# Kernel optimization log

Measured on AMD Instinct MI355X. Metric: run time of the kernel, lower is better.

The kernel has to match this reference:

```python
import jax, jax.numpy as jnp
import numpy as np

H = 1024  # hidden_size


def _cell(x, W, b):
    # x: [S, B, D_in]; W: [4H, D_in]; b: [4H]
    # One big batched matmul over all timesteps (no recurrence exists).
    gates = jnp.einsum('sbd,gd->sbg', x, W) + b  # [S, B, 4H]
    i, f, g, o = jnp.split(gates, 4, axis=-1)
    i = jax.nn.sigmoid(i)
    g = jnp.tanh(g)
    o = jax.nn.sigmoid(o)
    c = i * g
    h = o * jnp.tanh(c)
    return h, c


def setup_inputs() -> dict:
    key = jax.random.key(0)
    ks = jax.random.split(key, 9)
    S, B, D = 2048, 8, 1024
    s = 1.0 / np.sqrt(D)
    s2 = 1.0 / np.sqrt(2 * H)
    return {
        'x': jax.random.normal(ks[0], (S, B, D), dtype=jnp.float32),
        'W_f0': jax.random.uniform(ks[1], (4 * H, D), jnp.float32, -s, s),
        'b_f0': jax.random.uniform(ks[2], (4 * H,), jnp.float32, -s, s),
        'W_b0': jax.random.uniform(ks[3], (4 * H, D), jnp.float32, -s, s),
        'b_b0': jax.random.uniform(ks[4], (4 * H,), jnp.float32, -s, s),
        'W_f1': jax.random.uniform(ks[5], (4 * H, 2 * H), jnp.float32, -s2, s2),
        'b_f1': jax.random.uniform(ks[6], (4 * H,), jnp.float32, -s2, s2),
        'W_b1': jax.random.uniform(ks[7], (4 * H, 2 * H), jnp.float32, -s2, s2),
        'b_b1': jax.random.uniform(ks[8], (4 * H,), jnp.float32, -s2, s2),
    }


def reference(x, W_f0, b_f0, W_b0, b_b0, W_f1, b_f1, W_b1, b_b1):
    out = x
    h_ns, c_ns = [], []
    for (Wf, bf, Wb, bb) in [(W_f0, b_f0, W_b0, b_b0), (W_f1, b_f1, W_b1, b_b1)]:
        h_f, c_f = _cell(out, Wf, bf)  # forward direction
        h_b, c_b = _cell(out, Wb, bb)  # backward direction (same per-t math)
        out = jnp.concatenate([h_f, h_b], axis=-1)  # [S, B, 2H]
        # forward final state is at t = S-1; backward final state at t = 0
        h_ns += [h_f[-1], h_b[0]]
        c_ns += [c_f[-1], c_b[0]]
    h_n = jnp.stack(h_ns, axis=0)  # [num_layers*2, B, H]
    c_n = jnp.stack(c_ns, axis=0)
    return out, h_n, c_n
```

## Files before the change

### kernel.cpp

```cpp
#include <hip/hip_runtime.h>
#include <hip/hip_bf16.h>

#define S_LEN 2048
#define BATCH 8
#define HID   1024
#define NP    3072
#define MROWS 16384

using bf16x8 = __attribute__((ext_vector_type(8))) short;
using f32x4  = __attribute__((ext_vector_type(4))) float;

__device__ __forceinline__ unsigned short f2b(float f) {
  unsigned int u = __builtin_bit_cast(unsigned int, f);
  u += 0x7fffu + ((u >> 16) & 1u);
  return (unsigned short)(u >> 16);
}

__device__ __forceinline__ void load_lds16(const void* g, void* l) {
  __builtin_amdgcn_global_load_lds(
      (const __attribute__((address_space(1))) void*)g,
      (__attribute__((address_space(3))) void*)(unsigned int)(unsigned long long)l,
      16, 0, 0);
}

#define MEMFENCE asm volatile("" ::: "memory")
#define BARRIER  do { MEMFENCE; __builtin_amdgcn_s_barrier(); MEMFENCE; } while (0)

__global__ void cvt_f32_bf16(const float* __restrict__ in,
                             unsigned short* __restrict__ out, int n4) {
  int i = blockIdx.x * blockDim.x + threadIdx.x;
  if (i >= n4) return;
  const float4 v = reinterpret_cast<const float4*>(in)[i];
  ushort4 u;
  u.x = f2b(v.x); u.y = f2b(v.y); u.z = f2b(v.z); u.w = f2b(v.w);
  reinterpret_cast<ushort4*>(out)[i] = u;
}

__global__ void permute_w(const float* __restrict__ W,
                          unsigned short* __restrict__ Wp, int K) {
  long i = ((long)blockIdx.x * blockDim.x + threadIdx.x) * 4;
  int np = (int)(i / K);
  if (np >= NP) return;
  int k0 = (int)(i % K);
  int chunk = np / 48, rem = np % 48;
  int g3 = rem >> 4, hl = rem & 15;
  int og = (g3 == 0) ? 0 : (g3 == 1) ? 2 : 3;
  int n  = og * 1024 + chunk * 16 + hl;
  const float4 v = *reinterpret_cast<const float4*>(W + (long)n * K + k0);
  ushort4 u;
  u.x = f2b(v.x); u.y = f2b(v.y); u.z = f2b(v.z); u.w = f2b(v.w);
  *reinterpret_cast<ushort4*>(Wp + i) = u;
}

__global__ void permute_b(const float* __restrict__ b, float* __restrict__ bp) {
  int np = blockIdx.x * blockDim.x + threadIdx.x;
  if (np >= NP) return;
  int chunk = np / 48, rem = np % 48;
  int g3 = rem >> 4, hl = rem & 15;
  int og = (g3 == 0) ? 0 : (g3 == 1) ? 2 : 3;
  bp[np] = b[og * 1024 + chunk * 16 + hl];
}

template <int MODE>
__global__ void __launch_bounds__(256, 2)
lstm_gemm(const unsigned short* __restrict__ A,
          const unsigned short* __restrict__ WpF,
          const unsigned short* __restrict__ WpB,
          const float* __restrict__ bpF, const float* __restrict__ bpB,
          int K,
          unsigned short* __restrict__ out_bf, float* __restrict__ out_f,
          float* __restrict__ hn, float* __restrict__ cn) {
  __shared__ __align__(16) char lds[81920];

  const int dir = blockIdx.z;
  const unsigned short* __restrict__ Wp = dir ? WpB : WpF;
  const float* __restrict__ bp = dir ? bpB : bpF;
  const int bm = blockIdx.y;
  const int bn = blockIdx.x;

  const int tid  = threadIdx.x;
  const int wid  = tid >> 6;
  const int lane = tid & 63;
  const int wm   = wid >> 1;
  const int wn   = wid & 1;

  const int  nt = K >> 6;
  const long K2 = (long)K * 2;

  const int rlane = lane >> 3;
  const int cb    = (((lane & 7) ^ rlane) << 4);
  const char* Asrc = (const char*)A  + ((long)bm * 128 + rlane) * K2 + cb;
  const char* Bsrc = (const char*)Wp + ((long)bn * 192 + rlane) * K2 + cb;

  const int l15 = lane & 15;
  const int hi  = lane >> 4;
  const int c0  = ((hi ^ (l15 & 7)) << 4);
  const int aro = (wm * 64 + l15) * 128;
  const int bro = 16384 + (wn * 96 + l15) * 128;

  f32x4 acc[4][6];
  const f32x4 zero = {0.f, 0.f, 0.f, 0.f};
#pragma unroll
  for (int i = 0; i < 4; ++i)
#pragma unroll
    for (int j = 0; j < 6; ++j) acc[i][j] = zero;

  auto STAGE = [&](int t) {
    if (t >= nt) return;
    char* d = lds + (t & 1) * 40960;
    const long off = (long)t * 128;
#pragma unroll
    for (int s = 0; s < 4; ++s) {
      const int slot = s * 4 + wid;
      load_lds16(Asrc + (long)(slot * 8) * K2 + off, d + slot * 1024);
    }
#pragma unroll
    for (int s = 0; s < 6; ++s) {
      const int slot = s * 4 + wid;
      load_lds16(Bsrc + (long)(slot * 8) * K2 + off, d + 16384 + slot * 1024);
    }
  };

  STAGE(0);
  asm volatile("s_waitcnt vmcnt(0)" ::: "memory");
  BARRIER;

  for (int t = 0; t < nt; ++t) {
    STAGE(t + 1);

    const char* buf = lds + (t & 1) * 40960;
    bf16x8 a[4][2], b[6][2];
#pragma unroll
    for (int nf = 0; nf < 6; ++nf) {
      b[nf][0] = *(const bf16x8*)(buf + bro + nf * 2048 + c0);
      b[nf][1] = *(const bf16x8*)(buf + bro + nf * 2048 + (c0 ^ 64));
    }
#pragma unroll
    for (int mf = 0; mf < 4; ++mf) {
      a[mf][0] = *(const bf16x8*)(buf + aro + mf * 2048 + c0);
      a[mf][1] = *(const bf16x8*)(buf + aro + mf * 2048 + (c0 ^ 64));
    }

    __builtin_amdgcn_s_setprio(1);
#pragma unroll
    for (int mf = 0; mf < 4; ++mf)
#pragma unroll
      for (int nf = 0; nf < 6; ++nf) {
        acc[mf][nf] = __builtin_amdgcn_mfma_f32_16x16x32_bf16(
            a[mf][0], b[nf][0], acc[mf][nf], 0, 0, 0);
        acc[mf][nf] = __builtin_amdgcn_mfma_f32_16x16x32_bf16(
            a[mf][1], b[nf][1], acc[mf][nf], 0, 0, 0);
      }
    __builtin_amdgcn_s_setprio(0);

    asm volatile("s_waitcnt vmcnt(0)" ::: "memory");
    BARRIER;
  }

  const int col    = l15;
  const int rbase  = hi * 4;
  const int chunk0 = bn * 4 + wn * 2;
  const int Lidx   = MODE * 2 + dir;

#pragma unroll
  for (int hg = 0; hg < 2; ++hg) {
    const int chunk  = chunk0 + hg;
    const int h      = chunk * 16 + col;
    const int outcol = dir * HID + h;
    const float bi = bp[chunk * 48 + col];
    const float bg = bp[chunk * 48 + 16 + col];
    const float bo = bp[chunk * 48 + 32 + col];
#pragma unroll
    for (int mf = 0; mf < 4; ++mf) {
#pragma unroll
      for (int r = 0; r < 4; ++r) {
        const int m = bm * 128 + wm * 64 + mf * 16 + rbase + r;
        const float iv = acc[mf][hg * 3 + 0][r] + bi;
        const float gv = acc[mf][hg * 3 + 1][r] + bg;
        const float ov = acc[mf][hg * 3 + 2][r] + bo;
        const float is = 1.f / (1.f + __expf(-iv));
        const float gt = tanhf(gv);
        const float os = 1.f / (1.f + __expf(-ov));
        const float c  = is * gt;
        const float hv = os * tanhf(c);
        if (MODE == 0) {
          out_bf[(long)m * 2048 + outcol] = f2b(hv);
        } else {
          out_f[(long)m * 2048 + outcol] = hv;
        }
        const bool wst = (dir == 0) ? (m >= (S_LEN - 1) * BATCH) : (m < BATCH);
        if (wst) {
          const int b = (dir == 0) ? (m - (S_LEN - 1) * BATCH) : m;
          hn[((long)Lidx * BATCH + b) * HID + h] = hv;
          cn[((long)Lidx * BATCH + b) * HID + h] = c;
        }
      }
    }
  }
}

extern "C" void kernel_launch(void* const* d_in, const int* in_sizes, int n_in,
                              void* d_out, int out_size, void* d_ws, size_t ws_size,
                              hipStream_t stream) {
  const float* x    = (const float*)d_in[0];
  const float* W_f0 = (const float*)d_in[1];
  const float* b_f0 = (const float*)d_in[2];
  const float* W_b0 = (const float*)d_in[3];
  const float* b_b0 = (const float*)d_in[4];
  const float* W_f1 = (const float*)d_in[5];
  const float* b_f1 = (const float*)d_in[6];
  const float* W_b1 = (const float*)d_in[7];
  const float* b_b1 = (const float*)d_in[8];

  float* out = (float*)d_out;
  float* hn  = out + (long)MROWS * 2048;
  float* cn  = hn + 4 * BATCH * HID;

  unsigned short* x_bf  = (unsigned short*)d_ws;
  unsigned short* out1  = x_bf + (long)MROWS * 1024;
  unsigned short* wp_f0 = out1 + (long)MROWS * 2048;
  unsigned short* wp_b0 = wp_f0 + (long)NP * 1024;
  unsigned short* wp_f1 = wp_b0 + (long)NP * 1024;
  unsigned short* wp_b1 = wp_f1 + (long)NP * 2048;
  float* bp_f0 = (float*)(wp_b1 + (long)NP * 2048);
  float* bp_b0 = bp_f0 + NP;
  float* bp_f1 = bp_b0 + NP;
  float* bp_b1 = bp_f1 + NP;

  cvt_f32_bf16<<<16384, 256, 0, stream>>>(x, x_bf, MROWS * 1024 / 4);
  permute_w<<<3072, 256, 0, stream>>>(W_f0, wp_f0, 1024);
  permute_w<<<3072, 256, 0, stream>>>(W_b0, wp_b0, 1024);
  permute_w<<<6144, 256, 0, stream>>>(W_f1, wp_f1, 2048);
  permute_w<<<6144, 256, 0, stream>>>(W_b1, wp_b1, 2048);
  permute_b<<<12, 256, 0, stream>>>(b_f0, bp_f0);
  permute_b<<<12, 256, 0, stream>>>(b_b0, bp_b0);
  permute_b<<<12, 256, 0, stream>>>(b_f1, bp_f1);
  permute_b<<<12, 256, 0, stream>>>(b_b1, bp_b1);

  dim3 grid(NP / 192, MROWS / 128, 2);
  lstm_gemm<0><<<grid, 256, 0, stream>>>(x_bf, wp_f0, wp_b0, bp_f0, bp_b0, 1024,
                                         out1, nullptr, hn, cn);
  lstm_gemm<1><<<grid, 256, 0, stream>>>(out1, wp_f1, wp_b1, bp_f1, bp_b1, 2048,
                                         nullptr, out, hn, cn);
}
```

Baseline: 657.0 us.

## Prepack weights in MFMA fragment order and load B directly to registers

Weights are repacked into per-wave MFMA fragment layout so each lane loads its B operands straight from global memory into registers, double-buffered across two tiles. This bypasses LDS for B, shrinking shared memory from 80KB to 32KB, which removes LDS traffic and may allow more blocks per CU. The activation tanh is also replaced with an exp-based formula. The risks are higher register pressure from the two B register sets, less coalesced global reads of B since each wave fetches its own copy, and slightly different tanh accuracy.

```diff
diff --git a/kernel.cpp b/kernel.cpp
--- a/kernel.cpp
+++ b/kernel.cpp
@@ -14,6 +14,13 @@
   unsigned int u = __builtin_bit_cast(unsigned int, f);
   u += 0x7fffu + ((u >> 16) & 1u);
   return (unsigned short)(u >> 16);
+}
+
+__device__ __forceinline__ float sigf(float x) {
+  return 1.f / (1.f + __expf(-x));
+}
+__device__ __forceinline__ float tanh_f(float x) {
+  return 2.f / (1.f + __expf(-2.f * x)) - 1.f;
 }
 
 __device__ __forceinline__ void load_lds16(const void* g, void* l) {
@@ -36,20 +43,32 @@
   reinterpret_cast<ushort4*>(out)[i] = u;
 }
 
-__global__ void permute_w(const float* __restrict__ W,
-                          unsigned short* __restrict__ Wp, int K) {
-  long i = ((long)blockIdx.x * blockDim.x + threadIdx.x) * 4;
-  int np = (int)(i / K);
-  if (np >= NP) return;
-  int k0 = (int)(i % K);
-  int chunk = np / 48, rem = np % 48;
-  int g3 = rem >> 4, hl = rem & 15;
+__global__ void pack_w(const float* __restrict__ W,
+                       unsigned short* __restrict__ P, int K, int ntk) {
+  long id = (long)blockIdx.x * blockDim.x + threadIdx.x;
+  const long total = (long)NP * K / 8;
+  if (id >= total) return;
+  int l  = (int)(id & 63);
+  long r = id >> 6;
+  int kh = (int)(r & 1);   r >>= 1;
+  int nf = (int)(r % 6);   r /= 6;
+  int wn = (int)(r & 1);   r >>= 1;
+  int kt = (int)(r % ntk); r /= ntk;
+  int bn = (int)r;
+  int hg = nf / 3, g3 = nf % 3;
+  int chunk = bn * 4 + wn * 2 + hg;
   int og = (g3 == 0) ? 0 : (g3 == 1) ? 2 : 3;
-  int n  = og * 1024 + chunk * 16 + hl;
-  const float4 v = *reinterpret_cast<const float4*>(W + (long)n * K + k0);
-  ushort4 u;
-  u.x = f2b(v.x); u.y = f2b(v.y); u.z = f2b(v.z); u.w = f2b(v.w);
-  *reinterpret_cast<ushort4*>(Wp + i) = u;
+  int srow = og * 1024 + chunk * 16 + (l & 15);
+  int sk   = kt * 64 + kh * 32 + (l >> 4) * 8;
+  const float* s = W + (long)srow * K + sk;
+  const float4 v0 = *reinterpret_cast<const float4*>(s);
+  const float4 v1 = *reinterpret_cast<const float4*>(s + 4);
+  uint4 o;
+  o.x = (unsigned)f2b(v0.x) | ((unsigned)f2b(v0.y) << 16);
+  o.y = (unsigned)f2b(v0.z) | ((unsigned)f2b(v0.w) << 16);
+  o.z = (unsigned)f2b(v1.x) | ((unsigned)f2b(v1.y) << 16);
+  o.w = (unsigned)f2b(v1.z) | ((unsigned)f2b(v1.w) << 16);
+  *reinterpret_cast<uint4*>(P + id * 8) = o;
 }
 
 __global__ void permute_b(const float* __restrict__ b, float* __restrict__ bp) {
@@ -64,16 +83,16 @@
 template <int MODE>
 __global__ void __launch_bounds__(256, 2)
 lstm_gemm(const unsigned short* __restrict__ A,
-          const unsigned short* __restrict__ WpF,
-          const unsigned short* __restrict__ WpB,
+          const unsigned short* __restrict__ PF,
+          const unsigned short* __restrict__ PB,
           const float* __restrict__ bpF, const float* __restrict__ bpB,
           int K,
           unsigned short* __restrict__ out_bf, float* __restrict__ out_f,
           float* __restrict__ hn, float* __restrict__ cn) {
-  __shared__ __align__(16) char lds[81920];
+  __shared__ __align__(16) char lds[32768];
 
   const int dir = blockIdx.z;
-  const unsigned short* __restrict__ Wp = dir ? WpB : WpF;
+  const unsigned short* __restrict__ P = dir ? PB : PF;
   const float* __restrict__ bp = dir ? bpB : bpF;
   const int bm = blockIdx.y;
   const int bn = blockIdx.x;
@@ -89,14 +108,14 @@
 
   const int rlane = lane >> 3;
   const int cb    = (((lane & 7) ^ rlane) << 4);
-  const char* Asrc = (const char*)A  + ((long)bm * 128 + rlane) * K2 + cb;
-  const char* Bsrc = (const char*)Wp + ((long)bn * 192 + rlane) * K2 + cb;
+  const char* Asrc = (const char*)A + ((long)bm * 128 + rlane) * K2 + cb;
+
+  const char* Bbase = (const char*)P + (long)bn * nt * 24576 + wn * 12288 + lane * 16;
 
   const int l15 = lane & 15;
   const int hi  = lane >> 4;
   const int c0  = ((hi ^ (l15 & 7)) << 4);
   const int aro = (wm * 64 + l15) * 128;
-  const int bro = 16384 + (wn * 96 + l15) * 128;
 
   f32x4 acc[4][6];
   const f32x4 zero = {0.f, 0.f, 0.f, 0.f};
@@ -105,57 +124,68 @@
 #pragma unroll
     for (int j = 0; j < 6; ++j) acc[i][j] = zero;
 
-  auto STAGE = [&](int t) {
+  bf16x8 bE[6][2], bO[6][2];
+
+  auto STAGE_A = [&](int t) {
     if (t >= nt) return;
-    char* d = lds + (t & 1) * 40960;
+    char* d = lds + (t & 1) * 16384;
     const long off = (long)t * 128;
 #pragma unroll
     for (int s = 0; s < 4; ++s) {
       const int slot = s * 4 + wid;
       load_lds16(Asrc + (long)(slot * 8) * K2 + off, d + slot * 1024);
     }
-#pragma unroll
-    for (int s = 0; s < 6; ++s) {
-      const int slot = s * 4 + wid;
-      load_lds16(Bsrc + (long)(slot * 8) * K2 + off, d + 16384 + slot * 1024);
-    }
   };
 
-  STAGE(0);
-  asm volatile("s_waitcnt vmcnt(0)" ::: "memory");
+#define LOADB(breg, t)                                                       \
+  {                                                                          \
+    const char* p_ = Bbase + (long)(t) * 24576;                              \
+    _Pragma("unroll") for (int nf_ = 0; nf_ < 6; ++nf_)                      \
+      _Pragma("unroll") for (int kh_ = 0; kh_ < 2; ++kh_)                    \
+        breg[nf_][kh_] = *(const bf16x8*)(p_ + nf_ * 2048 + kh_ * 1024);     \
+  }
+
+  STAGE_A(0);
+  MEMFENCE;
+  LOADB(bE, 0);
+  MEMFENCE;
+  LOADB(bO, 1);
+  MEMFENCE;
+  asm volatile("s_waitcnt vmcnt(12)" ::: "memory");
   BARRIER;
 
-  for (int t = 0; t < nt; ++t) {
-    STAGE(t + 1);
-
-    const char* buf = lds + (t & 1) * 40960;
-    bf16x8 a[4][2], b[6][2];
-#pragma unroll
-    for (int nf = 0; nf < 6; ++nf) {
-      b[nf][0] = *(const bf16x8*)(buf + bro + nf * 2048 + c0);
-      b[nf][1] = *(const bf16x8*)(buf + bro + nf * 2048 + (c0 ^ 64));
-    }
-#pragma unroll
-    for (int mf = 0; mf < 4; ++mf) {
-      a[mf][0] = *(const bf16x8*)(buf + aro + mf * 2048 + c0);
-      a[mf][1] = *(const bf16x8*)(buf + aro + mf * 2048 + (c0 ^ 64));
-    }
-
-    __builtin_amdgcn_s_setprio(1);
-#pragma unroll
-    for (int mf = 0; mf < 4; ++mf)
-#pragma unroll
-      for (int nf = 0; nf < 6; ++nf) {
-        acc[mf][nf] = __builtin_amdgcn_mfma_f32_16x16x32_bf16(
-            a[mf][0], b[nf][0], acc[mf][nf], 0, 0, 0);
-        acc[mf][nf] = __builtin_amdgcn_mfma_f32_16x16x32_bf16(
-            a[mf][1], b[nf][1], acc[mf][nf], 0, 0, 0);
-      }
-    __builtin_amdgcn_s_setprio(0);
-
-    asm volatile("s_waitcnt vmcnt(0)" ::: "memory");
-    BARRIER;
-  }
+#define TILE(t, bcur)                                                        \
+  {                                                                          \
+    STAGE_A((t) + 1);                                                        \
+    MEMFENCE;                                                                \
+    const char* abuf = lds + ((t) & 1) * 16384 + aro;                        \
+    bf16x8 a[4][2];                                                          \
+    _Pragma("unroll") for (int mf = 0; mf < 4; ++mf) {                       \
+      a[mf][0] = *(const bf16x8*)(abuf + mf * 2048 + c0);                    \
+      a[mf][1] = *(const bf16x8*)(abuf + mf * 2048 + (c0 ^ 64));             \
+    }                                                                        \
+    __builtin_amdgcn_s_setprio(1);                                           \
+    _Pragma("unroll") for (int mf = 0; mf < 4; ++mf)                         \
+      _Pragma("unroll") for (int nf = 0; nf < 6; ++nf) {                     \
+        acc[mf][nf] = __builtin_amdgcn_mfma_f32_16x16x32_bf16(               \
+            a[mf][0], bcur[nf][0], acc[mf][nf], 0, 0, 0);                    \
+        acc[mf][nf] = __builtin_amdgcn_mfma_f32_16x16x32_bf16(               \
+            a[mf][1], bcur[nf][1], acc[mf][nf], 0, 0, 0);                    \
+      }                                                                      \
+    __builtin_amdgcn_s_setprio(0);                                           \
+    if ((t) + 2 < nt) { LOADB(bcur, (t) + 2); }                              \
+    MEMFENCE;                                                                \
+    if ((t) < nt - 2) { asm volatile("s_waitcnt vmcnt(12)" ::: "memory"); }  \
+    else              { asm volatile("s_waitcnt vmcnt(0)"  ::: "memory"); }  \
+    BARRIER;                                                                 \
+  }
+
+  for (int t = 0; t < nt; t += 2) {
+    TILE(t, bE);
+    TILE(t + 1, bO);
+  }
+#undef TILE
+#undef LOADB
 
   const int col    = l15;
   const int rbase  = hi * 4;
@@ -178,11 +208,11 @@
         const float iv = acc[mf][hg * 3 + 0][r] + bi;
         const float gv = acc[mf][hg * 3 + 1][r] + bg;
         const float ov = acc[mf][hg * 3 + 2][r] + bo;
-        const float is = 1.f / (1.f + __expf(-iv));
-        const float gt = tanhf(gv);
-        const float os = 1.f / (1.f + __expf(-ov));
+        const float is = sigf(iv);
+        const float gt = tanh_f(gv);
+        const float os = sigf(ov);
         const float c  = is * gt;
-        const float hv = os * tanhf(c);
+        const float hv = os * tanh_f(c);
         if (MODE == 0) {
           out_bf[(long)m * 2048 + outcol] = f2b(hv);
         } else {
@@ -228,10 +258,10 @@
   float* bp_b1 = bp_f1 + NP;
 
   cvt_f32_bf16<<<16384, 256, 0, stream>>>(x, x_bf, MROWS * 1024 / 4);
-  permute_w<<<3072, 256, 0, stream>>>(W_f0, wp_f0, 1024);
-  permute_w<<<3072, 256, 0, stream>>>(W_b0, wp_b0, 1024);
-  permute_w<<<6144, 256, 0, stream>>>(W_f1, wp_f1, 2048);
-  permute_w<<<6144, 256, 0, stream>>>(W_b1, wp_b1, 2048);
+  pack_w<<<1536, 256, 0, stream>>>(W_f0, wp_f0, 1024, 16);
+  pack_w<<<1536, 256, 0, stream>>>(W_b0, wp_b0, 1024, 16);
+  pack_w<<<3072, 256, 0, stream>>>(W_f1, wp_f1, 2048, 32);
+  pack_w<<<3072, 256, 0, stream>>>(W_b1, wp_b1, 2048, 32);
   permute_b<<<12, 256, 0, stream>>>(b_f0, bp_f0);
   permute_b<<<12, 256, 0, stream>>>(b_b0, bp_b0);
   permute_b<<<12, 256, 0, stream>>>(b_f1, bp_f1);
```

Measured after the change: 690.3 us. +5.1%, slower.

## Enlarge GEMM tile to 256x192 with 8 waves and 4-stage half-K pipeline

Applied to the files above, without the earlier changes.

Each workgroup now has 512 threads covering 256 rows. The load path changes: four waves load A and four load B into a four-slot ring of half-K LDS buffers, using split waitcnts and extra barriers so loads run ahead of the MFMA work. The LDS layout is re-swizzled so two rows share each 128-byte line. The epilogue swaps tanhf for an exp-based tanh. The aim is more B reuse per block and better load/compute overlap, at the cost of more LDS (112KB, so likely one block per CU), more barriers, and a slight loss of accuracy in tanh.

```diff
diff --git a/kernel.cpp b/kernel.cpp
--- a/kernel.cpp
+++ b/kernel.cpp
@@ -16,6 +16,13 @@
   return (unsigned short)(u >> 16);
 }
 
+__device__ __forceinline__ float sigf(float x) {
+  return 1.f / (1.f + __expf(-x));
+}
+__device__ __forceinline__ float tanh_f(float x) {
+  return 2.f / (1.f + __expf(-2.f * x)) - 1.f;
+}
+
 __device__ __forceinline__ void load_lds16(const void* g, void* l) {
   __builtin_amdgcn_global_load_lds(
       (const __attribute__((address_space(1))) void*)g,
@@ -25,6 +32,12 @@
 
 #define MEMFENCE asm volatile("" ::: "memory")
 #define BARRIER  do { MEMFENCE; __builtin_amdgcn_s_barrier(); MEMFENCE; } while (0)
+#define LGKM0    asm volatile("s_waitcnt lgkmcnt(0)" ::: "memory")
+#define WAITV(NA, NB) do {                                            \
+    if (wid < 4) asm volatile("s_waitcnt vmcnt(" #NA ")" ::: "memory"); \
+    else         asm volatile("s_waitcnt vmcnt(" #NB ")" ::: "memory"); \
+  } while (0)
+#define NOOP ((void)0)
 
 __global__ void cvt_f32_bf16(const float* __restrict__ in,
                              unsigned short* __restrict__ out, int n4) {
@@ -61,8 +74,22 @@
   bp[np] = b[og * 1024 + chunk * 16 + hl];
 }
 
+#define MFMAOP(a_, b_, c_) \
+  c_ = __builtin_amdgcn_mfma_f32_16x16x32_bf16(a_, b_, c_, 0, 0, 0)
+
+#define PH12(B0, B1, B2, N0, N1, N2) do {                     \
+    __builtin_amdgcn_s_setprio(1);                            \
+    MFMAOP(aa0, B0, acc[0][N0]); MFMAOP(aa1, B0, acc[1][N0]); \
+    MFMAOP(aa2, B0, acc[2][N0]); MFMAOP(aa3, B0, acc[3][N0]); \
+    MFMAOP(aa0, B1, acc[0][N1]); MFMAOP(aa1, B1, acc[1][N1]); \
+    MFMAOP(aa2, B1, acc[2][N1]); MFMAOP(aa3, B1, acc[3][N1]); \
+    MFMAOP(aa0, B2, acc[0][N2]); MFMAOP(aa1, B2, acc[1][N2]); \
+    MFMAOP(aa2, B2, acc[2][N2]); MFMAOP(aa3, B2, acc[3][N2]); \
+    __builtin_amdgcn_s_setprio(0);                            \
+  } while (0)
+
 template <int MODE>
-__global__ void __launch_bounds__(256, 2)
+__global__ void __launch_bounds__(512, 2)
 lstm_gemm(const unsigned short* __restrict__ A,
           const unsigned short* __restrict__ WpF,
           const unsigned short* __restrict__ WpB,
@@ -70,7 +97,7 @@
           int K,
           unsigned short* __restrict__ out_bf, float* __restrict__ out_f,
           float* __restrict__ hn, float* __restrict__ cn) {
-  __shared__ __align__(16) char lds[81920];
+  __shared__ __align__(16) char lds[114688];
 
   const int dir = blockIdx.z;
   const unsigned short* __restrict__ Wp = dir ? WpB : WpF;
@@ -87,16 +114,61 @@
   const int  nt = K >> 6;
   const long K2 = (long)K * 2;
 
-  const int rlane = lane >> 3;
-  const int cb    = (((lane & 7) ^ rlane) << 4);
-  const char* Asrc = (const char*)A  + ((long)bm * 128 + rlane) * K2 + cb;
-  const char* Bsrc = (const char*)Wp + ((long)bn * 192 + rlane) * K2 + cb;
+  const char* src[4];
+  int dst[4];
+  {
+    const int lline = lane >> 3;
+    const int lphys = lane & 7;
+    if (wid < 4) {
+#pragma unroll
+      for (int j = 0; j < 4; ++j) {
+        const int line0 = (wid * 4 + j) * 8;
+        const int line  = line0 + lline;
+        const int s     = lphys ^ (line & 7);
+        const long grow = (long)bm * 256 + line * 2 + (s >> 2);
+        src[j] = (const char*)A + grow * K2 + (s & 3) * 16;
+        dst[j] = line0 * 128;
+      }
+    } else {
+      const int bw = wid - 4;
+#pragma unroll
+      for (int j = 0; j < 3; ++j) {
+        const int line0 = (bw * 3 + j) * 8;
+        const int line  = line0 + lline;
+        const int s     = lphys ^ (line & 7);
+        const long grow = (long)bn * 192 + line * 2 + (s >> 2);
+        src[j] = (const char*)Wp + grow * K2 + (s & 3) * 16;
+        dst[j] = 16384 + line0 * 128;
+      }
+      src[3] = nullptr; dst[3] = 0;
+    }
+  }
+
+#define ISSUE(T, KH) do {                                        \
+    char* ibuf_ = lds + ((2 * (T) + (KH)) & 3) * 28672;          \
+    const long koff_ = (long)(T) * 128 + (KH) * 64;              \
+    if (wid < 4) {                                               \
+      _Pragma("unroll") for (int j_ = 0; j_ < 4; ++j_)           \
+        load_lds16(src[j_] + koff_, ibuf_ + dst[j_]);            \
+    } else {                                                     \
+      _Pragma("unroll") for (int j_ = 0; j_ < 3; ++j_)           \
+        load_lds16(src[j_] + koff_, ibuf_ + dst[j_]);            \
+    }                                                            \
+  } while (0)
 
   const int l15 = lane & 15;
   const int hi  = lane >> 4;
-  const int c0  = ((hi ^ (l15 & 7)) << 4);
-  const int aro = (wm * 64 + l15) * 128;
-  const int bro = 16384 + (wn * 96 + l15) * 128;
+  auto mkA = [&](int mf) {
+    const int r = wm * 64 + mf * 16 + l15, ln = r >> 1;
+    return ln * 128 + (((((r & 1) << 2) | hi) ^ (ln & 7)) * 16);
+  };
+  auto mkB = [&](int nf) {
+    const int r = wn * 96 + nf * 16 + l15, ln = r >> 1;
+    return 16384 + ln * 128 + (((((r & 1) << 2) | hi) ^ (ln & 7)) * 16);
+  };
+  const int aoff0 = mkA(0), aoff1 = mkA(1), aoff2 = mkA(2), aoff3 = mkA(3);
+  const int boff0 = mkB(0), boff1 = mkB(1), boff2 = mkB(2);
+  const int boff3 = mkB(3), boff4 = mkB(4), boff5 = mkB(5);
 
   f32x4 acc[4][6];
   const f32x4 zero = {0.f, 0.f, 0.f, 0.f};
@@ -105,57 +177,61 @@
 #pragma unroll
     for (int j = 0; j < 6; ++j) acc[i][j] = zero;
 
-  auto STAGE = [&](int t) {
-    if (t >= nt) return;
-    char* d = lds + (t & 1) * 40960;
-    const long off = (long)t * 128;
-#pragma unroll
-    for (int s = 0; s < 4; ++s) {
-      const int slot = s * 4 + wid;
-      load_lds16(Asrc + (long)(slot * 8) * K2 + off, d + slot * 1024);
-    }
-#pragma unroll
-    for (int s = 0; s < 6; ++s) {
-      const int slot = s * 4 + wid;
-      load_lds16(Bsrc + (long)(slot * 8) * K2 + off, d + 16384 + slot * 1024);
-    }
-  };
-
-  STAGE(0);
-  asm volatile("s_waitcnt vmcnt(0)" ::: "memory");
-  BARRIER;
-
-  for (int t = 0; t < nt; ++t) {
-    STAGE(t + 1);
-
-    const char* buf = lds + (t & 1) * 40960;
-    bf16x8 a[4][2], b[6][2];
-#pragma unroll
-    for (int nf = 0; nf < 6; ++nf) {
-      b[nf][0] = *(const bf16x8*)(buf + bro + nf * 2048 + c0);
-      b[nf][1] = *(const bf16x8*)(buf + bro + nf * 2048 + (c0 ^ 64));
-    }
-#pragma unroll
-    for (int mf = 0; mf < 4; ++mf) {
-      a[mf][0] = *(const bf16x8*)(buf + aro + mf * 2048 + c0);
-      a[mf][1] = *(const bf16x8*)(buf + aro + mf * 2048 + (c0 ^ 64));
-    }
-
-    __builtin_amdgcn_s_setprio(1);
-#pragma unroll
-    for (int mf = 0; mf < 4; ++mf)
-#pragma unroll
-      for (int nf = 0; nf < 6; ++nf) {
-        acc[mf][nf] = __builtin_amdgcn_mfma_f32_16x16x32_bf16(
-            a[mf][0], b[nf][0], acc[mf][nf], 0, 0, 0);
-        acc[mf][nf] = __builtin_amdgcn_mfma_f32_16x16x32_bf16(
-            a[mf][1], b[nf][1], acc[mf][nf], 0, 0, 0);
-      }
-    __builtin_amdgcn_s_setprio(0);
-
-    asm volatile("s_waitcnt vmcnt(0)" ::: "memory");
-    BARRIER;
+#define TILE_BODY(T, ISS1, ISS3, V1A, V1B, V3A, V3B) do {            \
+    const char* bh0_ = lds + (((2 * (T))    ) & 3) * 28672;          \
+    const char* bh1_ = lds + (((2 * (T)) + 1) & 3) * 28672;          \
+    bf16x8 aa0, aa1, aa2, aa3, bb0, bb1, bb2;                        \
+     \
+    ISS1;                                                            \
+    WAITV(V1A, V1B);                                                 \
+    BARRIER;                                                         \
+    aa0 = *(const bf16x8*)(bh0_ + aoff0);                            \
+    aa1 = *(const bf16x8*)(bh0_ + aoff1);                            \
+    aa2 = *(const bf16x8*)(bh0_ + aoff2);                            \
+    aa3 = *(const bf16x8*)(bh0_ + aoff3);                            \
+    bb0 = *(const bf16x8*)(bh0_ + boff0);                            \
+    bb1 = *(const bf16x8*)(bh0_ + boff1);                            \
+    bb2 = *(const bf16x8*)(bh0_ + boff2);                            \
+    PH12(bb0, bb1, bb2, 0, 1, 2);                                    \
+                                                            \
+    bb0 = *(const bf16x8*)(bh0_ + boff3);                            \
+    bb1 = *(const bf16x8*)(bh0_ + boff4);                            \
+    bb2 = *(const bf16x8*)(bh0_ + boff5);                            \
+    PH12(bb0, bb1, bb2, 3, 4, 5);                                    \
+    LGKM0; BARRIER;               \
+           \
+    ISS3;                                                            \
+    WAITV(V3A, V3B);                                                 \
+    BARRIER;                                                         \
+    aa0 = *(const bf16x8*)(bh1_ + aoff0);                            \
+    aa1 = *(const bf16x8*)(bh1_ + aoff1);                            \
+    aa2 = *(const bf16x8*)(bh1_ + aoff2);                            \
+    aa3 = *(const bf16x8*)(bh1_ + aoff3);                            \
+    bb0 = *(const bf16x8*)(bh1_ + boff0);                            \
+    bb1 = *(const bf16x8*)(bh1_ + boff1);                            \
+    bb2 = *(const bf16x8*)(bh1_ + boff2);                            \
+    PH12(bb0, bb1, bb2, 0, 1, 2);                                    \
+                                                            \
+    bb0 = *(const bf16x8*)(bh1_ + boff3);                            \
+    bb1 = *(const bf16x8*)(bh1_ + boff4);                            \
+    bb2 = *(const bf16x8*)(bh1_ + boff5);                            \
+    PH12(bb0, bb1, bb2, 3, 4, 5);                                    \
+    LGKM0; BARRIER;               \
+  } while (0)
+
+  ISSUE(0, 0); MEMFENCE;
+  ISSUE(0, 1); MEMFENCE;
+  ISSUE(1, 0); MEMFENCE;
+
+#pragma unroll 1
+  for (int t = 0; t < nt - 2; ++t) {
+    TILE_BODY(t, ISSUE(t + 1, 1), ISSUE(t + 2, 0), 12, 9, 12, 9);
   }
+  TILE_BODY(nt - 2, ISSUE(nt - 1, 1), NOOP, 12, 9, 8, 6);
+  TILE_BODY(nt - 1, NOOP, NOOP, 4, 3, 0, 0);
+
+#undef TILE_BODY
+#undef ISSUE
 
   const int col    = l15;
   const int rbase  = hi * 4;
@@ -174,15 +250,15 @@
     for (int mf = 0; mf < 4; ++mf) {
 #pragma unroll
       for (int r = 0; r < 4; ++r) {
-        const int m = bm * 128 + wm * 64 + mf * 16 + rbase + r;
+        const int m = bm * 256 + wm * 64 + mf * 16 + rbase + r;
         const float iv = acc[mf][hg * 3 + 0][r] + bi;
         const float gv = acc[mf][hg * 3 + 1][r] + bg;
         const float ov = acc[mf][hg * 3 + 2][r] + bo;
-        const float is = 1.f / (1.f + __expf(-iv));
-        const float gt = tanhf(gv);
-        const float os = 1.f / (1.f + __expf(-ov));
+        const float is = sigf(iv);
+        const float gt = tanh_f(gv);
+        const float os = sigf(ov);
         const float c  = is * gt;
-        const float hv = os * tanhf(c);
+        const float hv = os * tanh_f(c);
         if (MODE == 0) {
           out_bf[(long)m * 2048 + outcol] = f2b(hv);
         } else {
@@ -237,9 +313,9 @@
   permute_b<<<12, 256, 0, stream>>>(b_f1, bp_f1);
   permute_b<<<12, 256, 0, stream>>>(b_b1, bp_b1);
 
-  dim3 grid(NP / 192, MROWS / 128, 2);
-  lstm_gemm<0><<<grid, 256, 0, stream>>>(x_bf, wp_f0, wp_b0, bp_f0, bp_b0, 1024,
+  dim3 grid(NP / 192, MROWS / 256, 2);
+  lstm_gemm<0><<<grid, 512, 0, stream>>>(x_bf, wp_f0, wp_b0, bp_f0, bp_b0, 1024,
                                          out1, nullptr, hn, cn);
-  lstm_gemm<1><<<grid, 256, 0, stream>>>(out1, wp_f1, wp_b1, bp_f1, bp_b1, 2048,
+  lstm_gemm<1><<<grid, 512, 0, stream>>>(out1, wp_f1, wp_b1, bp_f1, bp_b1, 2048,
                                          nullptr, out, hn, cn);
 }
```

Result: slower. 773.4 us (+17.7%).
